# Kernel tuning notes

Hardware: AMD Instinct MI355X
Metric: run time of the kernel (lower is better)

## Reference

```python
import jax, jax.numpy as jnp
import numpy as np

N, E, G = 50000, 200000, 1000
EPS = 1e-5
NEG_SLOPE = 0.2


def setup_inputs() -> dict:
    key = jax.random.key(0)
    ks = jax.random.split(key, 24)
    p = lambda k, shape: jax.random.normal(k, shape, jnp.float32) * 0.05
    inp = {
        "x": jax.random.normal(ks[0], (N, 64), jnp.float32),
        "edge_index": jax.random.randint(ks[1], (2, E), 0, N, jnp.int32),
        "batch": jnp.sort(jax.random.randint(ks[2], (N,), 0, G, jnp.int32)),
        "solvent_fingerprint": jax.random.uniform(ks[3], (G, 128), jnp.float32),
        # GAT layer 1: 64 -> 4 heads x 128
        "W1": p(ks[4], (64, 512)), "a1_src": p(ks[5], (4, 128)), "a1_dst": p(ks[6], (4, 128)), "b1": jnp.zeros((512,), jnp.float32),
        "bn1_g": jnp.ones((512,), jnp.float32), "bn1_b": jnp.zeros((512,), jnp.float32),
        # GAT layer 2: 512 -> 4 heads x 256
        "W2": p(ks[7], (512, 1024)), "a2_src": p(ks[8], (4, 256)), "a2_dst": p(ks[9], (4, 256)), "b2": jnp.zeros((1024,), jnp.float32),
        "bn2_g": jnp.ones((1024,), jnp.float32), "bn2_b": jnp.zeros((1024,), jnp.float32),
        # GCN: 1024 -> 256
        "Wg": p(ks[10], (1024, 256)), "bg": jnp.zeros((256,), jnp.float32),
        "bn3_g": jnp.ones((256,), jnp.float32), "bn3_b": jnp.zeros((256,), jnp.float32),
        # MLP head
        "Ws": p(ks[11], (128, 128)), "bs": jnp.zeros((128,), jnp.float32),
        "Wf1": p(ks[12], (640, 128)), "bf1": jnp.zeros((128,), jnp.float32),
        "bnf_g": jnp.ones((128,), jnp.float32), "bnf_b": jnp.zeros((128,), jnp.float32),
        "Wf2": p(ks[13], (128, 1)), "bf2": jnp.zeros((1,), jnp.float32),
    }
    return inp


def _batchnorm(x, g, b):
    mu = x.mean(0)
    var = x.var(0)
    return (x - mu) * jax.lax.rsqrt(var + EPS) * g + b


def _gat(x, src, dst, W, a_src, a_dst, b, H, C):
    n = x.shape[0]
    h = (x @ W).reshape(n, H, C)                      # [N,H,C]
    al_s = (h * a_src).sum(-1)                        # [N,H]
    al_d = (h * a_dst).sum(-1)                        # [N,H]
    e = jax.nn.leaky_relu(al_s[src] + al_d[dst], NEG_SLOPE)   # [E,H]
    m = jax.ops.segment_max(e, dst, num_segments=n)
    ex = jnp.exp(e - m[dst])
    s = jax.ops.segment_sum(ex, dst, num_segments=n)
    alpha = ex / jnp.maximum(s[dst], 1e-16)
    out = jax.ops.segment_sum(h[src] * alpha[..., None], dst, num_segments=n)  # [N,H,C]
    return out.reshape(n, H * C) + b


def _gcn(x, src, dst, W, b):
    n = x.shape[0]
    h = x @ W
    deg = jax.ops.segment_sum(jnp.ones_like(dst, jnp.float32), dst, num_segments=n)
    dinv = jax.lax.rsqrt(jnp.maximum(deg, 1.0))
    norm = dinv[src] * dinv[dst]
    return jax.ops.segment_sum(h[src] * norm[:, None], dst, num_segments=n) + b


def reference(x, edge_index, batch, solvent_fingerprint,
              W1, a1_src, a1_dst, b1, bn1_g, bn1_b,
              W2, a2_src, a2_dst, b2, bn2_g, bn2_b,
              Wg, bg, bn3_g, bn3_b,
              Ws, bs, Wf1, bf1, bnf_g, bnf_b, Wf2, bf2):
    n = x.shape[0]
    loops = jnp.arange(n, dtype=edge_index.dtype)
    src = jnp.concatenate([edge_index[0], loops])
    dst = jnp.concatenate([edge_index[1], loops])

    h = _gat(x, src, dst, W1, a1_src, a1_dst, b1, 4, 128)
    h = jax.nn.relu(_batchnorm(h, bn1_g, bn1_b))
    h = _gat(h, src, dst, W2, a2_src, a2_dst, b2, 4, 256)
    h = jax.nn.relu(_batchnorm(h, bn2_g, bn2_b))
    h = _gcn(h, src, dst, Wg, bg)
    h = jax.nn.relu(_batchnorm(h, bn3_g, bn3_b))

    cnt = jax.ops.segment_sum(jnp.ones((n,), jnp.float32), batch, num_segments=G)
    gap = jax.ops.segment_sum(h, batch, num_segments=G) / jnp.maximum(cnt, 1.0)[:, None]
    gmp = jax.ops.segment_max(h, batch, num_segments=G)
    gmp = jnp.where(jnp.isfinite(gmp), gmp, 0.0)

    solv = jax.nn.relu(solvent_fingerprint @ Ws + bs)
    z = jnp.concatenate([gap, gmp, solv], axis=1)          # [G,640]
    z = jax.nn.relu(_batchnorm(z @ Wf1 + bf1, bnf_g, bnf_b))
    # dropout: identity in eval/deterministic reference
    return jax.nn.sigmoid(z @ Wf2 + bf2)
```

## Files before the change

kernel.cpp:

```cpp
#include <hip/hip_runtime.h>
#include <cmath>

#define LEAK 0.2f
#define BN_EPS 1e-5f

static inline int cdiv(long long a, long long b){ return (int)((a + b - 1) / b); }

typedef __attribute__((ext_vector_type(8))) short bf16x8;
typedef __attribute__((ext_vector_type(4))) float f32x4;

__device__ __forceinline__ float bf2f(unsigned short u){
    return __uint_as_float(((unsigned int)u) << 16);
}
__device__ __forceinline__ unsigned short f2bf(float f){
    unsigned int u = __float_as_uint(f);
    u += 0x7FFFu + ((u >> 16) & 1u);
    return (unsigned short)(u >> 16);
}

#define GLOAD_LDS16(gsrc, ldst) \
    __builtin_amdgcn_global_load_lds( \
        (const __attribute__((address_space(1))) unsigned int*)(gsrc), \
        (__attribute__((address_space(3))) unsigned int*)(ldst), 16, 0, 0)

__global__ __launch_bounds__(256) void gemm_mfma(
    const unsigned short* __restrict__ A, const unsigned short* __restrict__ Bt,
    unsigned short* __restrict__ D, int M, int K, int lda, int ldb, int ldc,
    int NX, int NYT)
{
    const int id = blockIdx.x;
    const int xcd = id & 7;
    const int j = id >> 3;
    const int bx = j % NX;
    const int by = (j / NX) * 8 + xcd;
    if (by >= NYT) return;

    __shared__ unsigned short As[128 * 64];
    __shared__ unsigned short Bs[128 * 64];
    const int t = threadIdx.x;
    const int row0 = by * 128, col0 = bx * 128;
    const int lane = t & 63, wv = t >> 6;
    const int wm = (wv >> 1) << 6, wn = (wv & 1) << 6;
    const int lm = lane & 15, lq = lane >> 4;

    const int sr  = t >> 3;
    const int scs = (t & 7) << 3;
    const int gsw = (((t & 7) ^ (sr & 7)) << 3);
    const unsigned short* ap[4];
    const unsigned short* bp[4];
    unsigned short* la[4];
    unsigned short* lb[4];
    #pragma unroll
    for (int q = 0; q < 4; ++q) {
        int r = sr + q * 32;
        int gra = row0 + r; if (gra >= M) gra = M - 1;
        ap[q] = A  + (size_t)gra * lda + gsw;
        bp[q] = Bt + (size_t)(col0 + r) * ldb + gsw;
        la[q] = &As[r * 64 + scs];
        lb[q] = &Bs[r * 64 + scs];
    }

    f32x4 acc[4][4] = {};
    const int rx = lm & 7;

    for (int k0 = 0; k0 < K; k0 += 64) {
        #pragma unroll
        for (int q = 0; q < 4; ++q) {
            GLOAD_LDS16(ap[q] + k0, la[q]);
            GLOAD_LDS16(bp[q] + k0, lb[q]);
        }
        __syncthreads();

        #pragma unroll
        for (int kk = 0; kk < 2; ++kk) {
            const int ck = (((kk << 2) + lq) ^ rx) << 3;
            bf16x8 af[4], bfr[4];
            #pragma unroll
            for (int mi = 0; mi < 4; ++mi)
                af[mi] = *(const bf16x8*)&As[(wm + mi * 16 + lm) * 64 + ck];
            #pragma unroll
            for (int ni = 0; ni < 4; ++ni)
                bfr[ni] = *(const bf16x8*)&Bs[(wn + ni * 16 + lm) * 64 + ck];
            #pragma unroll
            for (int mi = 0; mi < 4; ++mi)
                #pragma unroll
                for (int ni = 0; ni < 4; ++ni)
                    acc[mi][ni] = __builtin_amdgcn_mfma_f32_16x16x32_bf16(
                        af[mi], bfr[ni], acc[mi][ni], 0, 0, 0);
        }
        __syncthreads();
    }

    #pragma unroll
    for (int mi = 0; mi < 4; ++mi) {
        int row_b = row0 + wm + mi * 16 + lq * 4;
        #pragma unroll
        for (int ni = 0; ni < 4; ++ni) {
            int col = col0 + wn + ni * 16 + lm;
            #pragma unroll
            for (int r = 0; r < 4; ++r) {
                int row = row_b + r;
                if (row < M) D[(size_t)row * ldc + col] = f2bf(acc[mi][ni][r]);
            }
        }
    }
}

__global__ __launch_bounds__(256) void logits_valu(
    const unsigned short* __restrict__ A, const unsigned short* __restrict__ vat,
    float* __restrict__ C, int M, int K)
{
    __shared__ unsigned short vs[8 * 512];
    const int t = threadIdx.x;
    for (int i = t; i < K; i += 256)
        *(bf16x8*)&vs[i * 8] = *(const bf16x8*)(vat + (size_t)i * 8);
    __syncthreads();

    const int lane = t & 63;
    const int w = blockIdx.x * 4 + (t >> 6);
    const int Gl = K >> 3;
    const int rpw = 64 / Gl;
    const int sub = lane / Gl;
    const int li = lane - sub * Gl;
    long long row = (long long)w * rpw + sub;
    if (row >= M) return;

    bf16x8 hv = *(const bf16x8*)(A + row * K + li * 8);
    float hf[8];
    #pragma unroll
    for (int j = 0; j < 8; ++j) hf[j] = bf2f((unsigned short)hv[j]);

    float s[8];
    #pragma unroll
    for (int o = 0; o < 8; ++o) {
        bf16x8 v = *(const bf16x8*)&vs[o * K + li * 8];
        float acc = 0.f;
        #pragma unroll
        for (int j = 0; j < 8; ++j) acc += hf[j] * bf2f((unsigned short)v[j]);
        s[o] = acc;
    }
    for (int off = Gl >> 1; off; off >>= 1) {
        #pragma unroll
        for (int o = 0; o < 8; ++o) s[o] += __shfl_xor(s[o], off);
    }
    #pragma unroll
    for (int o = 0; o < 8; ++o)
        if (li == o) C[row * 8 + o] = s[o];
}

__global__ void convT(const float* __restrict__ W, unsigned short* __restrict__ Wt, int K, int Nc)
{
    int i = blockIdx.x * blockDim.x + threadIdx.x;
    if (i >= K * Nc) return;
    int k = i / Nc, n = i - k * Nc;
    Wt[(size_t)n * K + k] = f2bf(W[i]);
}

__global__ void conv_w1bd(const float* __restrict__ W, unsigned short* __restrict__ Wt)
{
    int i = blockIdx.x * blockDim.x + threadIdx.x;
    if (i >= 512 * 256) return;
    int o = i >> 8, k = i & 255;
    unsigned short v = 0;
    if ((k >> 6) == (o >> 7)) v = f2bf(W[(size_t)(k & 63) * 512 + o]);
    Wt[i] = v;
}

template<bool RELU>
__global__ __launch_bounds__(256) void gemm_small(
    const float* __restrict__ A, const float* __restrict__ B,
    const float* __restrict__ bias, float* __restrict__ C,
    int M, int K, int lda, int ldb, int ldc)
{
    __shared__ float As[2][640];
    const int t = threadIdx.x;
    const int r = t >> 7, c = t & 127;
    const int row0 = blockIdx.x * 2;
    for (int i = t; i < 2 * K; i += 256) {
        int rr = i / K, kk = i - rr * K;
        int gr = row0 + rr;
        As[rr][kk] = (gr < M) ? A[(size_t)gr * lda + kk] : 0.f;
    }
    __syncthreads();
    float acc0 = 0.f, acc1 = 0.f;
    for (int k = 0; k < K; k += 8) {
        float4 a0 = *reinterpret_cast<const float4*>(&As[r][k]);
        float4 a1 = *reinterpret_cast<const float4*>(&As[r][k + 4]);
        acc0 += a0.x * B[(size_t)(k + 0) * ldb + c];
        acc1 += a0.y * B[(size_t)(k + 1) * ldb + c];
        acc0 += a0.z * B[(size_t)(k + 2) * ldb + c];
        acc1 += a0.w * B[(size_t)(k + 3) * ldb + c];
        acc0 += a1.x * B[(size_t)(k + 4) * ldb + c];
        acc1 += a1.y * B[(size_t)(k + 5) * ldb + c];
        acc0 += a1.z * B[(size_t)(k + 6) * ldb + c];
        acc1 += a1.w * B[(size_t)(k + 7) * ldb + c];
    }
    int row = row0 + r;
    if (row < M) {
        float v = acc0 + acc1;
        if (bias) v += bias[c];
        if (RELU) v = fmaxf(v, 0.f);
        C[(size_t)row * ldc + c] = v;
    }
}

__global__ void compute_va_bf(const float* __restrict__ W, const float* __restrict__ a_s,
                              const float* __restrict__ a_d, unsigned short* __restrict__ vat,
                              int K, int HC, int C)
{
    int w = (int)(((long long)blockIdx.x * blockDim.x + threadIdx.x) >> 6);
    int lane = threadIdx.x & 63;
    if (w >= K * 4) return;
    int k = w >> 2, h = w & 3;
    const float* wp = W + (size_t)k * HC + h * C;
    const float* as = a_s + h * C;
    const float* ad = a_d + h * C;
    float s = 0.f, d = 0.f;
    for (int c = lane; c < C; c += 64) {
        float v = wp[c];
        s += v * as[c];
        d += v * ad[c];
    }
    #pragma unroll
    for (int off = 32; off; off >>= 1) {
        s += __shfl_down(s, off);
        d += __shfl_down(d, off);
    }
    if (lane == 0) {
        vat[(size_t)h * K + k] = f2bf(s);
        vat[(size_t)(4 + h) * K + k] = f2bf(d);
    }
}

__device__ __forceinline__ int e_src(const int* es, int E, int k){ return k < E ? es[k] : k - E; }
__device__ __forceinline__ int e_dst(const int* ed, int E, int k){ return k < E ? ed[k] : k - E; }

__global__ void fill_i32(int* __restrict__ p, int v, int n)
{
    int i = blockIdx.x * blockDim.x + threadIdx.x;
    if (i < n) p[i] = v;
}

__global__ void hist_dst(const int* __restrict__ ed, int E, int* __restrict__ cnt)
{
    int k = blockIdx.x * blockDim.x + threadIdx.x;
    if (k < E) atomicAdd(&cnt[ed[k]], 1);
}

__global__ __launch_bounds__(256) void scan_blk(const int* __restrict__ cnt,
                                                int* __restrict__ rowptr,
                                                int* __restrict__ bsums, int n)
{
    __shared__ int ts[256];
    const int t = threadIdx.x;
    const int i0 = blockIdx.x * 1024 + t * 4;
    int4 v = {0, 0, 0, 0};
    if (i0 + 3 < n) v = *reinterpret_cast<const int4*>(cnt + i0);
    else {
        if (i0 + 0 < n) v.x = cnt[i0 + 0];
        if (i0 + 1 < n) v.y = cnt[i0 + 1];
        if (i0 + 2 < n) v.z = cnt[i0 + 2];
        if (i0 + 3 < n) v.w = cnt[i0 + 3];
    }
    int lsum = v.x + v.y + v.z + v.w;
    ts[t] = lsum;
    __syncthreads();
    #pragma unroll
    for (int off = 1; off < 256; off <<= 1) {
        int u = (t >= off) ? ts[t - off] : 0;
        __syncthreads();
        ts[t] += u;
        __syncthreads();
    }
    int excl = ts[t] - lsum;
    if (i0 + 0 < n) rowptr[i0 + 0] = excl;
    if (i0 + 1 < n) rowptr[i0 + 1] = excl + v.x;
    if (i0 + 2 < n) rowptr[i0 + 2] = excl + v.x + v.y;
    if (i0 + 3 < n) rowptr[i0 + 3] = excl + v.x + v.y + v.z;
    if (t == 255) bsums[blockIdx.x] = ts[255];
}

__global__ __launch_bounds__(256) void scan_tops(int* __restrict__ bsums,
                                                 int* __restrict__ rowptr, int nb, int n)
{
    __shared__ int ts[256];
    const int t = threadIdx.x;
    int v = (t < nb) ? bsums[t] : 0;
    ts[t] = v;
    __syncthreads();
    #pragma unroll
    for (int off = 1; off < 256; off <<= 1) {
        int u = (t >= off) ? ts[t - off] : 0;
        __syncthreads();
        ts[t] += u;
        __syncthreads();
    }
    if (t < nb) bsums[t] = ts[t] - v;
    if (t == 255) rowptr[n] = ts[255];
}

__global__ void scan_add(int* __restrict__ rowptr, int* __restrict__ cursor,
                         const int* __restrict__ bsums, int n)
{
    int i = blockIdx.x * blockDim.x + threadIdx.x;
    if (i >= n) return;
    int r = rowptr[i] + bsums[i >> 10];
    rowptr[i] = r;
    cursor[i] = r;
}

__global__ void csr_scatter(const int* __restrict__ es, const int* __restrict__ ed,
                            int E, int Etot, int* __restrict__ cursor,
                            int* __restrict__ col, int* __restrict__ dstarr)
{
    int k = blockIdx.x * blockDim.x + threadIdx.x;
    if (k >= Etot) return;
    int sn = e_src(es, E, k), dn = e_dst(ed, E, k);
    int pos = atomicAdd(&cursor[dn], 1);
    col[pos] = sn;
    dstarr[pos] = dn;
}

__global__ void dinv_from_rowptr(const int* __restrict__ rowptr, float* __restrict__ dinv, int n)
{
    int i = blockIdx.x * blockDim.x + threadIdx.x;
    if (i < n) dinv[i] = rsqrtf(fmaxf((float)(rowptr[i + 1] - rowptr[i]), 1.f));
}

__global__ void grp_lb(const int* __restrict__ batch, int N, int G_, int* __restrict__ gptr)
{
    int g = blockIdx.x * blockDim.x + threadIdx.x;
    if (g > G_) return;
    if (g == G_) { gptr[G_] = N; return; }
    int lo = 0, hi = N;
    while (lo < hi) { int mid = (lo + hi) >> 1; if (batch[mid] < g) lo = mid + 1; else hi = mid; }
    gptr[g] = lo;
}

__global__ void edge_exp4(const int* __restrict__ col, const int* __restrict__ dstarr,
                          int Etot, const float* __restrict__ alsd, float* __restrict__ exq)
{
    int p = blockIdx.x * blockDim.x + threadIdx.x;
    if (p >= Etot) return;
    int sn = col[p], dn = dstarr[p];
    #pragma unroll
    for (int h = 0; h < 4; ++h) {
        float t = alsd[sn * 8 + h] + alsd[dn * 8 + 4 + h];
        t = (t >= 0.f) ? t : LEAK * t;
        exq[(size_t)h * Etot + p] = __expf(t);
    }
}

__global__ void gat_agg4_64(const int* __restrict__ rowptr, const int* __restrict__ col,
                            const unsigned short* __restrict__ xb,
                            const float* __restrict__ exq, int Etot,
                            unsigned short* __restrict__ agg, int N)
{
    int w = (int)(((long long)blockIdx.x * blockDim.x + threadIdx.x) >> 6);
    int lane = threadIdx.x & 63;
    if (w >= N) return;
    const float* ex0 = exq;
    const float* ex1 = exq + (size_t)Etot;
    const float* ex2 = exq + (size_t)2 * Etot;
    const float* ex3 = exq + (size_t)3 * Etot;
    int r0 = rowptr[w], r1 = rowptr[w + 1];
    float a0 = 0.f, a1 = 0.f, a2 = 0.f, a3 = 0.f;
    float s0 = 0.f, s1 = 0.f, s2 = 0.f, s3 = 0.f;
    int e = r0;
    for (; e + 1 < r1; e += 2) {
        int snA = col[e], snB = col[e + 1];
        float xA = bf2f(xb[(size_t)snA * 64 + lane]);
        float xB = bf2f(xb[(size_t)snB * 64 + lane]);
        float w0A = ex0[e], w0B = ex0[e + 1];
        float w1A = ex1[e], w1B = ex1[e + 1];
        float w2A = ex2[e], w2B = ex2[e + 1];
        float w3A = ex3[e], w3B = ex3[e + 1];
        a0 += w0A * xA + w0B * xB;  s0 += w0A + w0B;
        a1 += w1A * xA + w1B * xB;  s1 += w1A + w1B;
        a2 += w2A * xA + w2B * xB;  s2 += w2A + w2B;
        a3 += w3A * xA + w3B * xB;  s3 += w3A + w3B;
    }
    if (e < r1) {
        int sn = col[e];
        float xA = bf2f(xb[(size_t)sn * 64 + lane]);
        float w0 = ex0[e], w1 = ex1[e], w2 = ex2[e], w3 = ex3[e];
        a0 += w0 * xA; s0 += w0;
        a1 += w1 * xA; s1 += w1;
        a2 += w2 * xA; s2 += w2;
        a3 += w3 * xA; s3 += w3;
    }
    unsigned short* op = agg + (size_t)w * 256 + lane;
    op[0]   = f2bf(a0 / fmaxf(s0, 1e-16f));
    op[64]  = f2bf(a1 / fmaxf(s1, 1e-16f));
    op[128] = f2bf(a2 / fmaxf(s2, 1e-16f));
    op[192] = f2bf(a3 / fmaxf(s3, 1e-16f));
}

__global__ void gat_gather512_bf2(const int* __restrict__ rowptr, const int* __restrict__ col,
                                  const unsigned short* __restrict__ h, int ldh,
                                  const float* __restrict__ exq0, const float* __restrict__ exq1,
                                  unsigned short* __restrict__ out, int N)
{
    int w = (int)(((long long)blockIdx.x * blockDim.x + threadIdx.x) >> 6);
    int lane = threadIdx.x & 63;
    if (w >= N) return;
    int r0 = rowptr[w], r1 = rowptr[w + 1];
    float s0 = 0.f, s1 = 0.f;
    float a00=0.f,a01=0.f,a02=0.f,a03=0.f;
    float a10=0.f,a11=0.f,a12=0.f,a13=0.f;
    int e = r0;
    for (; e + 1 < r1; e += 2) {
        int sA = col[e], sB = col[e + 1];
        float w0A = exq0[e], w0B = exq0[e + 1];
        float w1A = exq1[e], w1B = exq1[e + 1];
        const unsigned short* pA = h + (size_t)sA * ldh + lane * 4;
        const unsigned short* pB = h + (size_t)sB * ldh + lane * 4;
        ushort4 hA0 = *reinterpret_cast<const ushort4*>(pA);
        ushort4 hA1 = *reinterpret_cast<const ushort4*>(pA + 256);
        ushort4 hB0 = *reinterpret_cast<const ushort4*>(pB);
        ushort4 hB1 = *reinterpret_cast<const ushort4*>(pB + 256);
        s0 += w0A + w0B; s1 += w1A + w1B;
        a00 += bf2f(hA0.x) * w0A + bf2f(hB0.x) * w0B;
        a01 += bf2f(hA0.y) * w0A + bf2f(hB0.y) * w0B;
        a02 += bf2f(hA0.z) * w0A + bf2f(hB0.z) * w0B;
        a03 += bf2f(hA0.w) * w0A + bf2f(hB0.w) * w0B;
        a10 += bf2f(hA1.x) * w1A + bf2f(hB1.x) * w1B;
        a11 += bf2f(hA1.y) * w1A + bf2f(hB1.y) * w1B;
        a12 += bf2f(hA1.z) * w1A + bf2f(hB1.z) * w1B;
        a13 += bf2f(hA1.w) * w1A + bf2f(hB1.w) * w1B;
    }
    if (e < r1) {
        int sA = col[e];
        float w0A = exq0[e], w1A = exq1[e];
        const unsigned short* pA = h + (size_t)sA * ldh + lane * 4;
        ushort4 hA0 = *reinterpret_cast<const ushort4*>(pA);
        ushort4 hA1 = *reinterpret_cast<const ushort4*>(pA + 256);
        s0 += w0A; s1 += w1A;
        a00 += bf2f(hA0.x) * w0A; a01 += bf2f(hA0.y) * w0A;
        a02 += bf2f(hA0.z) * w0A; a03 += bf2f(hA0.w) * w0A;
        a10 += bf2f(hA1.x) * w1A; a11 += bf2f(hA1.y) * w1A;
        a12 += bf2f(hA1.z) * w1A; a13 += bf2f(hA1.w) * w1A;
    }
    float i0 = 1.f / fmaxf(s0, 1e-16f);
    float i1 = 1.f / fmaxf(s1, 1e-16f);
    ushort4 o0, o1;
    o0.x = f2bf(a00 * i0); o0.y = f2bf(a01 * i0);
    o0.z = f2bf(a02 * i0); o0.w = f2bf(a03 * i0);
    o1.x = f2bf(a10 * i1); o1.y = f2bf(a11 * i1);
    o1.z = f2bf(a12 * i1); o1.w = f2bf(a13 * i1);
    unsigned short* op = out + (size_t)w * 512 + lane * 4;
    *reinterpret_cast<ushort4*>(op)       = o0;
    *reinterpret_cast<ushort4*>(op + 256) = o1;
}

__global__ void gcn_gather256(const int* __restrict__ rowptr, const int* __restrict__ col,
                              const unsigned short* __restrict__ h,
                              const float* __restrict__ dinv,
                              unsigned short* __restrict__ out, int N)
{
    int w = (int)(((long long)blockIdx.x * blockDim.x + threadIdx.x) >> 6);
    int lane = threadIdx.x & 63;
    if (w >= N) return;
    int r0 = rowptr[w], r1 = rowptr[w + 1];
    float a0 = 0.f, a1 = 0.f, a2 = 0.f, a3 = 0.f;
    int e = r0;
    for (; e + 1 < r1; e += 2) {
        int sn0 = col[e], sn1 = col[e + 1];
        float w0 = dinv[sn0], w1 = dinv[sn1];
        ushort4 hv0 = *reinterpret_cast<const ushort4*>(h + (size_t)sn0 * 256 + lane * 4);
        ushort4 hv1 = *reinterpret_cast<const ushort4*>(h + (size_t)sn1 * 256 + lane * 4);
        a0 += bf2f(hv0.x) * w0 + bf2f(hv1.x) * w1;
        a1 += bf2f(hv0.y) * w0 + bf2f(hv1.y) * w1;
        a2 += bf2f(hv0.z) * w0 + bf2f(hv1.z) * w1;
        a3 += bf2f(hv0.w) * w0 + bf2f(hv1.w) * w1;
    }
    if (e < r1) {
        int sn = col[e];
        float wv = dinv[sn];
        ushort4 hv = *reinterpret_cast<const ushort4*>(h + (size_t)sn * 256 + lane * 4);
        a0 += bf2f(hv.x) * wv; a1 += bf2f(hv.y) * wv;
        a2 += bf2f(hv.z) * wv; a3 += bf2f(hv.w) * wv;
    }
    float dn = dinv[w];
    ushort4 o;
    o.x = f2bf(a0 * dn); o.y = f2bf(a1 * dn);
    o.z = f2bf(a2 * dn); o.w = f2bf(a3 * dn);
    *reinterpret_cast<ushort4*>(out + (size_t)w * 256 + lane * 4) = o;
}

template<int D>
__global__ __launch_bounds__(256) void bn_part(
    const float* __restrict__ x, float* __restrict__ ps, float* __restrict__ pq,
    int M, int Y)
{
    constexpr int DG = D / 4;
    constexpr int P  = 256 / DG;
    const int t = threadIdx.x;
    const int cg = t % DG, ph = t / DG;
    const int y = blockIdx.y;
    const int rows_per = (M + Y - 1) / Y;
    const int r0 = y * rows_per;
    const int r1 = min(r0 + rows_per, M);
    float s0=0,s1=0,s2=0,s3=0,q0=0,q1=0,q2=0,q3=0;
    for (int r = r0 + ph; r < r1; r += P) {
        float4 v = *reinterpret_cast<const float4*>(x + (size_t)r * D + cg * 4);
        s0+=v.x; s1+=v.y; s2+=v.z; s3+=v.w;
        q0+=v.x*v.x; q1+=v.y*v.y; q2+=v.z*v.z; q3+=v.w*v.w;
    }
    __shared__ float ls[P][D];
    __shared__ float lq[P][D];
    ls[ph][cg*4+0]=s0; ls[ph][cg*4+1]=s1; ls[ph][cg*4+2]=s2; ls[ph][cg*4+3]=s3;
    lq[ph][cg*4+0]=q0; lq[ph][cg*4+1]=q1; lq[ph][cg*4+2]=q2; lq[ph][cg*4+3]=q3;
    __syncthreads();
    if (ph == 0) {
        #pragma unroll
        for (int j = 0; j < 4; ++j) {
            float ss = 0.f, qq = 0.f;
            #pragma unroll
            for (int p = 0; p < P; ++p) { ss += ls[p][cg*4+j]; qq += lq[p][cg*4+j]; }
            ps[(size_t)y * D + cg*4 + j] = ss;
            pq[(size_t)y * D + cg*4 + j] = qq;
        }
    }
}

template<int D>
__global__ __launch_bounds__(256) void bn_part_bf(
    const unsigned short* __restrict__ x, int ldx,
    float* __restrict__ ps, float* __restrict__ pq, int M, int Y)
{
    constexpr int DG = D / 4;
    constexpr int P  = 256 / DG;
    const int t = threadIdx.x;
    const int cg = t % DG, ph = t / DG;
    const int y = blockIdx.y;
    const int rows_per = (M + Y - 1) / Y;
    const int r0 = y * rows_per;
    const int r1 = min(r0 + rows_per, M);
    float s0=0,s1=0,s2=0,s3=0,q0=0,q1=0,q2=0,q3=0;
    for (int r = r0 + ph; r < r1; r += P) {
        ushort4 u = *reinterpret_cast<const ushort4*>(x + (size_t)r * ldx + cg * 4);
        float vx = bf2f(u.x), vy = bf2f(u.y), vz = bf2f(u.z), vw = bf2f(u.w);
        s0+=vx; s1+=vy; s2+=vz; s3+=vw;
        q0+=vx*vx; q1+=vy*vy; q2+=vz*vz; q3+=vw*vw;
    }
    __shared__ float ls[P][D];
    __shared__ float lq[P][D];
    ls[ph][cg*4+0]=s0; ls[ph][cg*4+1]=s1; ls[ph][cg*4+2]=s2; ls[ph][cg*4+3]=s3;
    lq[ph][cg*4+0]=q0; lq[ph][cg*4+1]=q1; lq[ph][cg*4+2]=q2; lq[ph][cg*4+3]=q3;
    __syncthreads();
    if (ph == 0) {
        #pragma unroll
        for (int j = 0; j < 4; ++j) {
            float ss = 0.f, qq = 0.f;
            #pragma unroll
            for (int p = 0; p < P; ++p) { ss += ls[p][cg*4+j]; qq += lq[p][cg*4+j]; }
            ps[(size_t)y * D + cg*4 + j] = ss;
            pq[(size_t)y * D + cg*4 + j] = qq;
        }
    }
}

template<int D>
__global__ __launch_bounds__(256) void bn_reduce_fin(
    const float* __restrict__ ps, const float* __restrict__ pq,
    const float* __restrict__ g, const float* __restrict__ b,
    float* __restrict__ scale, float* __restrict__ shift, int Y, float invM)
{
    const int t = threadIdx.x;
    const int cl = t & 63;
    const int c = blockIdx.x * 64 + cl;
    const int ph = t >> 6;
    float s = 0.f, q = 0.f;
    for (int y = ph; y < Y; y += 4) {
        s += ps[(size_t)y * D + c];
        q += pq[(size_t)y * D + c];
    }
    __shared__ float ls[4][64];
    __shared__ float lq[4][64];
    ls[ph][cl] = s; lq[ph][cl] = q;
    __syncthreads();
    if (ph == 0) {
        s = ls[0][cl] + ls[1][cl] + ls[2][cl] + ls[3][cl];
        q = lq[0][cl] + lq[1][cl] + lq[2][cl] + lq[3][cl];
        float mu = s * invM;
        float var = q * invM - mu * mu;
        float rs = rsqrtf(var + BN_EPS) * g[c];
        scale[c] = rs;
        shift[c] = b[c] - mu * rs;
    }
}

__global__ void bn_apply_bfbf(const unsigned short* __restrict__ x,
                              const float* __restrict__ scale, const float* __restrict__ shift,
                              unsigned short* __restrict__ dst, int total4, int Cb4,
                              int ldx, int ldd)
{
    int i = blockIdx.x * blockDim.x + threadIdx.x;
    if (i >= total4) return;
    int r = i / Cb4, c4 = (i - r * Cb4) * 4;
    ushort4 u = *reinterpret_cast<const ushort4*>(x + (size_t)r * ldx + c4);
    float4 sc = *reinterpret_cast<const float4*>(scale + c4);
    float4 sh = *reinterpret_cast<const float4*>(shift + c4);
    ushort4 o;
    o.x = f2bf(fmaxf(bf2f(u.x) * sc.x + sh.x, 0.f));
    o.y = f2bf(fmaxf(bf2f(u.y) * sc.y + sh.y, 0.f));
    o.z = f2bf(fmaxf(bf2f(u.z) * sc.z + sh.z, 0.f));
    o.w = f2bf(fmaxf(bf2f(u.w) * sc.w + sh.w, 0.f));
    *reinterpret_cast<ushort4*>(dst + (size_t)r * ldd + c4) = o;
}

__global__ void conv_f2b4(const float* __restrict__ src, unsigned short* __restrict__ dst, int n4)
{
    int i = blockIdx.x * blockDim.x + threadIdx.x;
    if (i >= n4) return;
    float4 v = *reinterpret_cast<const float4*>(src + (size_t)i * 4);
    ushort4 o = { f2bf(v.x), f2bf(v.y), f2bf(v.z), f2bf(v.w) };
    *reinterpret_cast<ushort4*>(dst + (size_t)i * 4) = o;
}

__global__ __launch_bounds__(256) void pool_gather_bn(const unsigned short* __restrict__ h,
                                                      const float* __restrict__ scale,
                                                      const float* __restrict__ shift,
                                                      const int* __restrict__ gptr,
                                                      float* __restrict__ z, int G_)
{
    int g = blockIdx.x;
    int c = threadIdx.x;
    int r0 = gptr[g], r1 = gptr[g + 1];
    float sc = scale[c], sh = shift[c];
    float s = 0.f, m = 0.f;
    int i = r0;
    for (; i + 1 < r1; i += 2) {
        float v0 = fmaxf(bf2f(h[(size_t)i * 256 + c]) * sc + sh, 0.f);
        float v1 = fmaxf(bf2f(h[(size_t)(i + 1) * 256 + c]) * sc + sh, 0.f);
        s += v0 + v1;
        m = fmaxf(m, fmaxf(v0, v1));
    }
    if (i < r1) {
        float v = fmaxf(bf2f(h[(size_t)i * 256 + c]) * sc + sh, 0.f);
        s += v;
        m = fmaxf(m, v);
    }
    float cnt = fmaxf((float)(r1 - r0), 1.f);
    z[(size_t)g * 640 + c] = s / cnt;
    z[(size_t)g * 640 + 256 + c] = m;
}

__global__ void final_head_bn(const float* __restrict__ f1,
                              const float* __restrict__ scale, const float* __restrict__ shift,
                              const float* __restrict__ Wf2, const float* __restrict__ bf2,
                              float* __restrict__ out, int G_)
{
    int w = (int)(((long long)blockIdx.x * blockDim.x + threadIdx.x) >> 6);
    int lane = threadIdx.x & 63;
    if (w >= G_) return;
    float s = 0.f;
    #pragma unroll
    for (int q = 0; q < 2; ++q) {
        int c = lane + q * 64;
        float v = fmaxf(f1[(size_t)w * 128 + c] * scale[c] + shift[c], 0.f);
        s += v * Wf2[c];
    }
    #pragma unroll
    for (int off = 32; off; off >>= 1) s += __shfl_down(s, off);
    if (lane == 0) out[w] = 1.f / (1.f + __expf(-(s + bf2[0])));
}

__global__ void sentinel(float* __restrict__ out, int n, float v)
{
    int i = blockIdx.x * blockDim.x + threadIdx.x;
    if (i < n) out[i] = v;
}

extern "C" void kernel_launch(void* const* d_in, const int* in_sizes, int n_in,
                              void* d_out, int out_size, void* d_ws, size_t ws_size,
                              hipStream_t stream)
{
    const float* x    = (const float*)d_in[0];
    const int*   ei   = (const int*)d_in[1];
    const int*   batch= (const int*)d_in[2];
    const float* sfp  = (const float*)d_in[3];
    const float* W1   = (const float*)d_in[4];
    const float* a1s  = (const float*)d_in[5];
    const float* a1d  = (const float*)d_in[6];
    const float* bn1g = (const float*)d_in[8];
    const float* bn1b = (const float*)d_in[9];
    const float* W2   = (const float*)d_in[10];
    const float* a2s  = (const float*)d_in[11];
    const float* a2d  = (const float*)d_in[12];
    const float* bn2g = (const float*)d_in[14];
    const float* bn2b = (const float*)d_in[15];
    const float* Wg   = (const float*)d_in[16];
    const float* bn3g = (const float*)d_in[18];
    const float* bn3b = (const float*)d_in[19];
    const float* Wsm  = (const float*)d_in[20];
    const float* bsm  = (const float*)d_in[21];
    const float* Wf1  = (const float*)d_in[22];
    const float* bnfg = (const float*)d_in[24];
    const float* bnfb = (const float*)d_in[25];
    const float* Wf2  = (const float*)d_in[26];
    const float* bf2  = (const float*)d_in[27];
    float* outp = (float*)d_out;

    const int N    = in_sizes[0] / 64;
    const int E    = in_sizes[1] / 2;
    const int G_   = in_sizes[3] / 128;
    const int Etot = E + N;
    const int* esrc = ei;
    const int* edst = ei + E;
    const int YB = 256;
    const int NB = cdiv(N, 1024);
    const int NYT = cdiv(N, 128);
    const int NYT8 = cdiv(NYT, 8) * 8;

    float* ws = (float*)d_ws;
    size_t off = 0;
    float* accA  = ws + off; off += (size_t)N * 256;
    float* h3acc = ws + off; off += (size_t)N * 256;
    unsigned short* g1b   = (unsigned short*)accA;
    unsigned short* g3b   = (unsigned short*)accA;
    unsigned short* h2all = (unsigned short*)accA;
    unsigned short* R1 = (unsigned short*)(ws + off); off += (size_t)N * 256;
    unsigned short* o1n = R1;
    unsigned short* hb  = (unsigned short*)(ws + off); off += (size_t)N * 128;
    unsigned short* xb  = (unsigned short*)(ws + off); off += (size_t)N * 32;
    float* alsd = ws + off; off += (size_t)N * 8;
    float* dinv = ws + off; off += N;
    float* bsc = ws + off; off += 1024;
    float* bsh = ws + off; off += 1024;
    float* ps  = ws + off; off += (size_t)YB * 512;
    float* pq  = ws + off; off += (size_t)YB * 512;
    float* z   = ws + off; off += (size_t)G_ * 640;
    float* f1  = ws + off; off += (size_t)G_ * 128;
    int* rowptr = (int*)(ws + off); off += (size_t)(N + 1);
    int* colc   = (int*)(ws + off); off += (size_t)Etot;
    int* dstarr = (int*)(ws + off); off += (size_t)Etot;
    float* exq  = ws + off; off += (size_t)Etot * 4;
    int* gptr   = (int*)(ws + off); off += (size_t)(G_ + 1);
    int* bsums  = (int*)(ws + off); off += 256;
    off = (off + 3) & ~(size_t)3;
    unsigned short* vat1 = (unsigned short*)(ws + off); off += 128 * 64 / 2;
    unsigned short* vat2 = (unsigned short*)(ws + off); off += 128 * 512 / 2;
    unsigned short* W1bdt = (unsigned short*)(ws + off); off += 512 * 256 / 2;
    unsigned short* W2t = (unsigned short*)(ws + off); off += 512 * 1024 / 2;
    unsigned short* Wgt = (unsigned short*)(ws + off); off += 1024 * 256 / 2;
    int* cursor = (int*)alsd;
    size_t need = off * 4;
    if (ws_size < need) {
        sentinel<<<cdiv(out_size, 256), 256, 0, stream>>>(outp, out_size, (float)(ws_size >> 20));
        return;
    }

    const int BLK = 256;
    dim3 blk(BLK);

    conv_w1bd<<<cdiv(512 * 256, BLK), blk, 0, stream>>>(W1, W1bdt);
    convT<<<cdiv(512 * 1024, BLK), blk, 0, stream>>>(W2, W2t, 512, 1024);
    convT<<<cdiv(1024 * 256, BLK), blk, 0, stream>>>(Wg, Wgt, 1024, 256);
    conv_f2b4<<<cdiv((long long)N * 16, BLK), blk, 0, stream>>>(x, xb, N * 16);
    compute_va_bf<<<cdiv(64 * 4 * 64, BLK), blk, 0, stream>>>(W1, a1s, a1d, vat1, 64, 512, 128);
    compute_va_bf<<<cdiv(512 * 4 * 64, BLK), blk, 0, stream>>>(W2, a2s, a2d, vat2, 512, 1024, 256);

    fill_i32<<<cdiv(N, BLK), blk, 0, stream>>>(cursor, 1, N);
    hist_dst<<<cdiv(E, BLK), blk, 0, stream>>>(edst, E, cursor);
    scan_blk<<<NB, blk, 0, stream>>>(cursor, rowptr, bsums, N);
    scan_tops<<<1, blk, 0, stream>>>(bsums, rowptr, NB, N);
    scan_add<<<cdiv(N, BLK), blk, 0, stream>>>(rowptr, cursor, bsums, N);
    csr_scatter<<<cdiv(Etot, BLK), blk, 0, stream>>>(esrc, edst, E, Etot, cursor, colc, dstarr);
    dinv_from_rowptr<<<cdiv(N, BLK), blk, 0, stream>>>(rowptr, dinv, N);
    grp_lb<<<cdiv(G_ + 1, BLK), blk, 0, stream>>>(batch, N, G_, gptr);

    logits_valu<<<cdiv(N, 32), blk, 0, stream>>>(xb, vat1, alsd, N, 64);
    edge_exp4<<<cdiv(Etot, BLK), blk, 0, stream>>>(colc, dstarr, Etot, alsd, exq);
    gat_agg4_64<<<cdiv((long long)N * 64, BLK), blk, 0, stream>>>(
        rowptr, colc, xb, exq, Etot, hb, N);
    gemm_mfma<<<NYT8 * 4, blk, 0, stream>>>(hb, W1bdt, g1b, N, 256, 256, 256, 512, 4, NYT);
    { dim3 g(1, YB); bn_part_bf<512><<<g, blk, 0, stream>>>(g1b, 512, ps, pq, N, YB); }
    bn_reduce_fin<512><<<8, blk, 0, stream>>>(ps, pq, bn1g, bn1b, bsc, bsh, YB, 1.f / N);
    bn_apply_bfbf<<<cdiv((long long)N * 128, BLK), blk, 0, stream>>>(
        g1b, bsc, bsh, o1n, N * 128, 128, 512, 512);

    logits_valu<<<cdiv(N, 4), blk, 0, stream>>>(o1n, vat2, alsd, N, 512);
    edge_exp4<<<cdiv(Etot, BLK), blk, 0, stream>>>(colc, dstarr, Etot, alsd, exq);

    gemm_mfma<<<NYT8 * 8, blk, 0, stream>>>(o1n, W2t, h2all, N, 512, 512, 512, 1024, 8, NYT);
    for (int pr = 0; pr < 2; ++pr) {
        gat_gather512_bf2<<<cdiv((long long)N * 64, BLK), blk, 0, stream>>>(
            rowptr, colc, h2all + pr * 512, 1024,
            exq + (size_t)(2 * pr) * Etot, exq + (size_t)(2 * pr + 1) * Etot, R1, N);
        { dim3 g(1, YB); bn_part_bf<512><<<g, blk, 0, stream>>>(R1, 512, ps, pq, N, YB); }
        bn_reduce_fin<512><<<8, blk, 0, stream>>>(ps, pq, bn2g + pr * 512, bn2b + pr * 512,
                                                  bsc + pr * 512, bsh + pr * 512, YB, 1.f / N);
        bn_apply_bfbf<<<cdiv((long long)N * 128, BLK), blk, 0, stream>>>(
            R1, bsc + pr * 512, bsh + pr * 512, h2all + pr * 512, N * 128, 128, 512, 1024);
    }
    gemm_mfma<<<NYT8 * 2, blk, 0, stream>>>(h2all, Wgt, hb, N, 1024, 1024, 1024, 256, 2, NYT);

    gcn_gather256<<<cdiv((long long)N * 64, BLK), blk, 0, stream>>>(
        rowptr, colc, hb, dinv, g3b, N);
    { dim3 g(1, YB); bn_part_bf<256><<<g, blk, 0, stream>>>(g3b, 256, ps, pq, N, YB); }
    bn_reduce_fin<256><<<4, blk, 0, stream>>>(ps, pq, bn3g, bn3b, bsc, bsh, YB, 1.f / N);

    pool_gather_bn<<<G_, blk, 0, stream>>>(g3b, bsc, bsh, gptr, z, G_);

    gemm_small<true><<<cdiv(G_, 2), blk, 0, stream>>>(
        sfp, Wsm, bsm, z + 512, G_, 128, 128, 128, 640);

    gemm_small<false><<<cdiv(G_, 2), blk, 0, stream>>>(
        z, Wf1, nullptr, f1, G_, 640, 640, 128, 128);
    { dim3 g(1, YB); bn_part<128><<<g, blk, 0, stream>>>(f1, ps, pq, G_, YB); }
    bn_reduce_fin<128><<<2, blk, 0, stream>>>(ps, pq, bnfg, bnfb, bsc, bsh, YB, 1.f / G_);
    final_head_bn<<<cdiv((long long)G_ * 64, BLK), blk, 0, stream>>>(
        f1, bsc, bsh, Wf2, bf2, outp, G_);
}
```

Baseline: 840.0 us.

## Fuse prep kernels and compute GAT edge weights inline in gathers

Merges the weight conversions, x conversion, attention-vector precompute, cursor fill and group-bound search into one multi-role prep kernel, and merges the CSR scatter with the dinv computation. It removes the edge_exp4 kernels and the exq/dstarr buffers, so the gather kernels recompute leaky-relu and exp per edge from the alsd logits. This cuts launch count and global traffic for edge weights, but adds redundant exp work per lane and drops the two-edge unrolling in the gather loops.

```diff
diff --git a/kernel.cpp b/kernel.cpp
--- a/kernel.cpp
+++ b/kernel.cpp
@@ -16,6 +16,11 @@
     unsigned int u = __float_as_uint(f);
     u += 0x7FFFu + ((u >> 16) & 1u);
     return (unsigned short)(u >> 16);
+}
+__device__ __forceinline__ float edge_ex(float s, float d){
+    float t = s + d;
+    t = (t >= 0.f) ? t : LEAK * t;
+    return __expf(t);
 }
 
 #define GLOAD_LDS16(gsrc, ldst) \
@@ -148,22 +153,97 @@
         if (li == o) C[row * 8 + o] = s[o];
 }
 
-__global__ void convT(const float* __restrict__ W, unsigned short* __restrict__ Wt, int K, int Nc)
-{
-    int i = blockIdx.x * blockDim.x + threadIdx.x;
-    if (i >= K * Nc) return;
-    int k = i / Nc, n = i - k * Nc;
-    Wt[(size_t)n * K + k] = f2bf(W[i]);
-}
-
-__global__ void conv_w1bd(const float* __restrict__ W, unsigned short* __restrict__ Wt)
-{
-    int i = blockIdx.x * blockDim.x + threadIdx.x;
-    if (i >= 512 * 256) return;
-    int o = i >> 8, k = i & 255;
-    unsigned short v = 0;
-    if ((k >> 6) == (o >> 7)) v = f2bf(W[(size_t)(k & 63) * 512 + o]);
-    Wt[i] = v;
+__global__ __launch_bounds__(256) void prep_all(
+    const float* __restrict__ W1, const float* __restrict__ W2,
+    const float* __restrict__ Wg, const float* __restrict__ x,
+    const float* __restrict__ a1s, const float* __restrict__ a1d,
+    const float* __restrict__ a2s, const float* __restrict__ a2d,
+    const int* __restrict__ batch,
+    unsigned short* __restrict__ W1bdt, unsigned short* __restrict__ W2t,
+    unsigned short* __restrict__ Wgt, unsigned short* __restrict__ xb,
+    unsigned short* __restrict__ vat1, unsigned short* __restrict__ vat2,
+    int* __restrict__ cursor, int* __restrict__ gptr,
+    int N, int G_,
+    int c0, int c1, int c2, int c3, int c4, int c5, int c6)
+{
+    const int t = threadIdx.x;
+    const int bid = blockIdx.x;
+    if (bid < c0) {
+        int i = bid * 256 + t;
+        int o = i >> 8, k = i & 255;
+        unsigned short v = 0;
+        if ((k >> 6) == (o >> 7)) v = f2bf(W1[(size_t)(k & 63) * 512 + o]);
+        W1bdt[i] = v;
+    } else if (bid < c1) {
+        int i = (bid - c0) * 256 + t;
+        int k = i >> 10, n = i & 1023;
+        W2t[(size_t)n * 512 + k] = f2bf(W2[i]);
+    } else if (bid < c2) {
+        int i = (bid - c1) * 256 + t;
+        int k = i >> 8, n = i & 255;
+        Wgt[(size_t)n * 1024 + k] = f2bf(Wg[i]);
+    } else if (bid < c3) {
+        int i = (bid - c2) * 256 + t;
+        if (i < N * 16) {
+            float4 v = *reinterpret_cast<const float4*>(x + (size_t)i * 4);
+            ushort4 o = { f2bf(v.x), f2bf(v.y), f2bf(v.z), f2bf(v.w) };
+            *reinterpret_cast<ushort4*>(xb + (size_t)i * 4) = o;
+        }
+    } else if (bid < c4) {
+        int w = (((bid - c3) * 256 + t) >> 6);
+        int lane = t & 63;
+        int k = w >> 2, h = w & 3;
+        const float* wp = W1 + (size_t)k * 512 + h * 128;
+        const float* as = a1s + h * 128;
+        const float* ad = a1d + h * 128;
+        float s = 0.f, d = 0.f;
+        for (int c = lane; c < 128; c += 64) {
+            float v = wp[c];
+            s += v * as[c];
+            d += v * ad[c];
+        }
+        #pragma unroll
+        for (int off = 32; off; off >>= 1) {
+            s += __shfl_down(s, off);
+            d += __shfl_down(d, off);
+        }
+        if (lane == 0) {
+            vat1[(size_t)h * 64 + k] = f2bf(s);
+            vat1[(size_t)(4 + h) * 64 + k] = f2bf(d);
+        }
+    } else if (bid < c5) {
+        int w = (((bid - c4) * 256 + t) >> 6);
+        int lane = t & 63;
+        int k = w >> 2, h = w & 3;
+        const float* wp = W2 + (size_t)k * 1024 + h * 256;
+        const float* as = a2s + h * 256;
+        const float* ad = a2d + h * 256;
+        float s = 0.f, d = 0.f;
+        for (int c = lane; c < 256; c += 64) {
+            float v = wp[c];
+            s += v * as[c];
+            d += v * ad[c];
+        }
+        #pragma unroll
+        for (int off = 32; off; off >>= 1) {
+            s += __shfl_down(s, off);
+            d += __shfl_down(d, off);
+        }
+        if (lane == 0) {
+            vat2[(size_t)h * 512 + k] = f2bf(s);
+            vat2[(size_t)(4 + h) * 512 + k] = f2bf(d);
+        }
+    } else if (bid < c6) {
+        int i = (bid - c5) * 256 + t;
+        if (i < N) cursor[i] = 1;
+    } else {
+        int g = (bid - c6) * 256 + t;
+        if (g > G_) return;
+        if (g == G_) { gptr[G_] = N; return; }
+        int lo = 0, hi = N;
+        while (lo < hi) { int mid = (lo + hi) >> 1; if (batch[mid] < g) lo = mid + 1; else hi = mid; }
+        gptr[g] = lo;
+    }
 }
 
 template<bool RELU>
@@ -204,42 +284,8 @@
     }
 }
 
-__global__ void compute_va_bf(const float* __restrict__ W, const float* __restrict__ a_s,
-                              const float* __restrict__ a_d, unsigned short* __restrict__ vat,
-                              int K, int HC, int C)
-{
-    int w = (int)(((long long)blockIdx.x * blockDim.x + threadIdx.x) >> 6);
-    int lane = threadIdx.x & 63;
-    if (w >= K * 4) return;
-    int k = w >> 2, h = w & 3;
-    const float* wp = W + (size_t)k * HC + h * C;
-    const float* as = a_s + h * C;
-    const float* ad = a_d + h * C;
-    float s = 0.f, d = 0.f;
-    for (int c = lane; c < C; c += 64) {
-        float v = wp[c];
-        s += v * as[c];
-        d += v * ad[c];
-    }
-    #pragma unroll
-    for (int off = 32; off; off >>= 1) {
-        s += __shfl_down(s, off);
-        d += __shfl_down(d, off);
-    }
-    if (lane == 0) {
-        vat[(size_t)h * K + k] = f2bf(s);
-        vat[(size_t)(4 + h) * K + k] = f2bf(d);
-    }
-}
-
 __device__ __forceinline__ int e_src(const int* es, int E, int k){ return k < E ? es[k] : k - E; }
 __device__ __forceinline__ int e_dst(const int* ed, int E, int k){ return k < E ? ed[k] : k - E; }
-
-__global__ void fill_i32(int* __restrict__ p, int v, int n)
-{
-    int i = blockIdx.x * blockDim.x + threadIdx.x;
-    if (i < n) p[i] = v;
-}
 
 __global__ void hist_dst(const int* __restrict__ ed, int E, int* __restrict__ cnt)
 {
@@ -309,85 +355,50 @@
     cursor[i] = r;
 }
 
-__global__ void csr_scatter(const int* __restrict__ es, const int* __restrict__ ed,
-                            int E, int Etot, int* __restrict__ cursor,
-                            int* __restrict__ col, int* __restrict__ dstarr)
-{
-    int k = blockIdx.x * blockDim.x + threadIdx.x;
-    if (k >= Etot) return;
-    int sn = e_src(es, E, k), dn = e_dst(ed, E, k);
-    int pos = atomicAdd(&cursor[dn], 1);
-    col[pos] = sn;
-    dstarr[pos] = dn;
-}
-
-__global__ void dinv_from_rowptr(const int* __restrict__ rowptr, float* __restrict__ dinv, int n)
-{
-    int i = blockIdx.x * blockDim.x + threadIdx.x;
-    if (i < n) dinv[i] = rsqrtf(fmaxf((float)(rowptr[i + 1] - rowptr[i]), 1.f));
-}
-
-__global__ void grp_lb(const int* __restrict__ batch, int N, int G_, int* __restrict__ gptr)
-{
-    int g = blockIdx.x * blockDim.x + threadIdx.x;
-    if (g > G_) return;
-    if (g == G_) { gptr[G_] = N; return; }
-    int lo = 0, hi = N;
-    while (lo < hi) { int mid = (lo + hi) >> 1; if (batch[mid] < g) lo = mid + 1; else hi = mid; }
-    gptr[g] = lo;
-}
-
-__global__ void edge_exp4(const int* __restrict__ col, const int* __restrict__ dstarr,
-                          int Etot, const float* __restrict__ alsd, float* __restrict__ exq)
-{
-    int p = blockIdx.x * blockDim.x + threadIdx.x;
-    if (p >= Etot) return;
-    int sn = col[p], dn = dstarr[p];
-    #pragma unroll
-    for (int h = 0; h < 4; ++h) {
-        float t = alsd[sn * 8 + h] + alsd[dn * 8 + 4 + h];
-        t = (t >= 0.f) ? t : LEAK * t;
-        exq[(size_t)h * Etot + p] = __expf(t);
+__global__ void csr_scatter_dinv(const int* __restrict__ es, const int* __restrict__ ed,
+                                 int E, int Etot, int* __restrict__ cursor,
+                                 int* __restrict__ col,
+                                 const int* __restrict__ rowptr,
+                                 float* __restrict__ dinv, int N, int NBsc)
+{
+    const int bid = blockIdx.x;
+    const int t = threadIdx.x;
+    if (bid < NBsc) {
+        int k = bid * 256 + t;
+        if (k >= Etot) return;
+        int sn = e_src(es, E, k), dn = e_dst(ed, E, k);
+        int pos = atomicAdd(&cursor[dn], 1);
+        col[pos] = sn;
+    } else {
+        int i = (bid - NBsc) * 256 + t;
+        if (i < N) dinv[i] = rsqrtf(fmaxf((float)(rowptr[i + 1] - rowptr[i]), 1.f));
     }
 }
 
 __global__ void gat_agg4_64(const int* __restrict__ rowptr, const int* __restrict__ col,
                             const unsigned short* __restrict__ xb,
-                            const float* __restrict__ exq, int Etot,
+                            const float* __restrict__ alsd,
                             unsigned short* __restrict__ agg, int N)
 {
     int w = (int)(((long long)blockIdx.x * blockDim.x + threadIdx.x) >> 6);
     int lane = threadIdx.x & 63;
     if (w >= N) return;
-    const float* ex0 = exq;
-    const float* ex1 = exq + (size_t)Etot;
-    const float* ex2 = exq + (size_t)2 * Etot;
-    const float* ex3 = exq + (size_t)3 * Etot;
+    float4 dt = *reinterpret_cast<const float4*>(alsd + (size_t)w * 8 + 4);
     int r0 = rowptr[w], r1 = rowptr[w + 1];
     float a0 = 0.f, a1 = 0.f, a2 = 0.f, a3 = 0.f;
     float s0 = 0.f, s1 = 0.f, s2 = 0.f, s3 = 0.f;
-    int e = r0;
-    for (; e + 1 < r1; e += 2) {
-        int snA = col[e], snB = col[e + 1];
-        float xA = bf2f(xb[(size_t)snA * 64 + lane]);
-        float xB = bf2f(xb[(size_t)snB * 64 + lane]);
-        float w0A = ex0[e], w0B = ex0[e + 1];
-        float w1A = ex1[e], w1B = ex1[e + 1];
-        float w2A = ex2[e], w2B = ex2[e + 1];
-        float w3A = ex3[e], w3B = ex3[e + 1];
-        a0 += w0A * xA + w0B * xB;  s0 += w0A + w0B;
-        a1 += w1A * xA + w1B * xB;  s1 += w1A + w1B;
-        a2 += w2A * xA + w2B * xB;  s2 += w2A + w2B;
-        a3 += w3A * xA + w3B * xB;  s3 += w3A + w3B;
-    }
-    if (e < r1) {
+    for (int e = r0; e < r1; ++e) {
         int sn = col[e];
+        float4 st = *reinterpret_cast<const float4*>(alsd + (size_t)sn * 8);
+        float e0 = edge_ex(st.x, dt.x);
+        float e1 = edge_ex(st.y, dt.y);
+        float e2 = edge_ex(st.z, dt.z);
+        float e3 = edge_ex(st.w, dt.w);
         float xA = bf2f(xb[(size_t)sn * 64 + lane]);
-        float w0 = ex0[e], w1 = ex1[e], w2 = ex2[e], w3 = ex3[e];
-        a0 += w0 * xA; s0 += w0;
-        a1 += w1 * xA; s1 += w1;
-        a2 += w2 * xA; s2 += w2;
-        a3 += w3 * xA; s3 += w3;
+        a0 += e0 * xA; s0 += e0;
+        a1 += e1 * xA; s1 += e1;
+        a2 += e2 * xA; s2 += e2;
+        a3 += e3 * xA; s3 += e3;
     }
     unsigned short* op = agg + (size_t)w * 256 + lane;
     op[0]   = f2bf(a0 / fmaxf(s0, 1e-16f));
@@ -396,58 +407,37 @@
     op[192] = f2bf(a3 / fmaxf(s3, 1e-16f));
 }
 
-__global__ void gat_gather512_bf2(const int* __restrict__ rowptr, const int* __restrict__ col,
-                                  const unsigned short* __restrict__ h, int ldh,
-                                  const float* __restrict__ exq0, const float* __restrict__ exq1,
-                                  unsigned short* __restrict__ out, int N)
+__global__ void gat_gather512_ex(const int* __restrict__ rowptr, const int* __restrict__ col,
+                                 const unsigned short* __restrict__ h, int ldh,
+                                 const float* __restrict__ alsd, int pr,
+                                 unsigned short* __restrict__ out, int N)
 {
     int w = (int)(((long long)blockIdx.x * blockDim.x + threadIdx.x) >> 6);
     int lane = threadIdx.x & 63;
     if (w >= N) return;
+    float2 dt = *reinterpret_cast<const float2*>(alsd + (size_t)w * 8 + 4 + 2 * pr);
     int r0 = rowptr[w], r1 = rowptr[w + 1];
     float s0 = 0.f, s1 = 0.f;
     float a00=0.f,a01=0.f,a02=0.f,a03=0.f;
     float a10=0.f,a11=0.f,a12=0.f,a13=0.f;
-    int e = r0;
-    for (; e + 1 < r1; e += 2) {
-        int sA = col[e], sB = col[e + 1];
-        float w0A = exq0[e], w0B = exq0[e + 1];
-        float w1A = exq1[e], w1B = exq1[e + 1];
-        const unsigned short* pA = h + (size_t)sA * ldh + lane * 4;
-        const unsigned short* pB = h + (size_t)sB * ldh + lane * 4;
-        ushort4 hA0 = *reinterpret_cast<const ushort4*>(pA);
-        ushort4 hA1 = *reinterpret_cast<const ushort4*>(pA + 256);
-        ushort4 hB0 = *reinterpret_cast<const ushort4*>(pB);
-        ushort4 hB1 = *reinterpret_cast<const ushort4*>(pB + 256);
-        s0 += w0A + w0B; s1 += w1A + w1B;
-        a00 += bf2f(hA0.x) * w0A + bf2f(hB0.x) * w0B;
-        a01 += bf2f(hA0.y) * w0A + bf2f(hB0.y) * w0B;
-        a02 += bf2f(hA0.z) * w0A + bf2f(hB0.z) * w0B;
-        a03 += bf2f(hA0.w) * w0A + bf2f(hB0.w) * w0B;
-        a10 += bf2f(hA1.x) * w1A + bf2f(hB1.x) * w1B;
-        a11 += bf2f(hA1.y) * w1A + bf2f(hB1.y) * w1B;
-        a12 += bf2f(hA1.z) * w1A + bf2f(hB1.z) * w1B;
-        a13 += bf2f(hA1.w) * w1A + bf2f(hB1.w) * w1B;
-    }
-    if (e < r1) {
-        int sA = col[e];
-        float w0A = exq0[e], w1A = exq1[e];
-        const unsigned short* pA = h + (size_t)sA * ldh + lane * 4;
-        ushort4 hA0 = *reinterpret_cast<const ushort4*>(pA);
-        ushort4 hA1 = *reinterpret_cast<const ushort4*>(pA + 256);
-        s0 += w0A; s1 += w1A;
-        a00 += bf2f(hA0.x) * w0A; a01 += bf2f(hA0.y) * w0A;
-        a02 += bf2f(hA0.z) * w0A; a03 += bf2f(hA0.w) * w0A;
-        a10 += bf2f(hA1.x) * w1A; a11 += bf2f(hA1.y) * w1A;
-        a12 += bf2f(hA1.z) * w1A; a13 += bf2f(hA1.w) * w1A;
+    for (int e = r0; e < r1; ++e) {
+        int sn = col[e];
+        float2 st = *reinterpret_cast<const float2*>(alsd + (size_t)sn * 8 + 2 * pr);
+        float e0 = edge_ex(st.x, dt.x);
+        float e1 = edge_ex(st.y, dt.y);
+        const unsigned short* p = h + (size_t)sn * ldh + lane * 4;
+        ushort4 h0 = *reinterpret_cast<const ushort4*>(p);
+        ushort4 h1 = *reinterpret_cast<const ushort4*>(p + 256);
+        s0 += e0; s1 += e1;
+        a00 += bf2f(h0.x) * e0; a01 += bf2f(h0.y) * e0;
+        a02 += bf2f(h0.z) * e0; a03 += bf2f(h0.w) * e0;
+        a10 += bf2f(h1.x) * e1; a11 += bf2f(h1.y) * e1;
+        a12 += bf2f(h1.z) * e1; a13 += bf2f(h1.w) * e1;
     }
     float i0 = 1.f / fmaxf(s0, 1e-16f);
     float i1 = 1.f / fmaxf(s1, 1e-16f);
-    ushort4 o0, o1;
-    o0.x = f2bf(a00 * i0); o0.y = f2bf(a01 * i0);
-    o0.z = f2bf(a02 * i0); o0.w = f2bf(a03 * i0);
-    o1.x = f2bf(a10 * i1); o1.y = f2bf(a11 * i1);
-    o1.z = f2bf(a12 * i1); o1.w = f2bf(a13 * i1);
+    ushort4 o0 = { f2bf(a00*i0), f2bf(a01*i0), f2bf(a02*i0), f2bf(a03*i0) };
+    ushort4 o1 = { f2bf(a10*i1), f2bf(a11*i1), f2bf(a12*i1), f2bf(a13*i1) };
     unsigned short* op = out + (size_t)w * 512 + lane * 4;
     *reinterpret_cast<ushort4*>(op)       = o0;
     *reinterpret_cast<ushort4*>(op + 256) = o1;
@@ -608,15 +598,6 @@
     o.z = f2bf(fmaxf(bf2f(u.z) * sc.z + sh.z, 0.f));
     o.w = f2bf(fmaxf(bf2f(u.w) * sc.w + sh.w, 0.f));
     *reinterpret_cast<ushort4*>(dst + (size_t)r * ldd + c4) = o;
-}
-
-__global__ void conv_f2b4(const float* __restrict__ src, unsigned short* __restrict__ dst, int n4)
-{
-    int i = blockIdx.x * blockDim.x + threadIdx.x;
-    if (i >= n4) return;
-    float4 v = *reinterpret_cast<const float4*>(src + (size_t)i * 4);
-    ushort4 o = { f2bf(v.x), f2bf(v.y), f2bf(v.z), f2bf(v.w) };
-    *reinterpret_cast<ushort4*>(dst + (size_t)i * 4) = o;
 }
 
 __global__ __launch_bounds__(256) void pool_gather_bn(const unsigned short* __restrict__ h,
@@ -735,8 +716,6 @@
     float* f1  = ws + off; off += (size_t)G_ * 128;
     int* rowptr = (int*)(ws + off); off += (size_t)(N + 1);
     int* colc   = (int*)(ws + off); off += (size_t)Etot;
-    int* dstarr = (int*)(ws + off); off += (size_t)Etot;
-    float* exq  = ws + off; off += (size_t)Etot * 4;
     int* gptr   = (int*)(ws + off); off += (size_t)(G_ + 1);
     int* bsums  = (int*)(ws + off); off += 256;
     off = (off + 3) & ~(size_t)3;
@@ -755,26 +734,30 @@
     const int BLK = 256;
     dim3 blk(BLK);
 
-    conv_w1bd<<<cdiv(512 * 256, BLK), blk, 0, stream>>>(W1, W1bdt);
-    convT<<<cdiv(512 * 1024, BLK), blk, 0, stream>>>(W2, W2t, 512, 1024);
-    convT<<<cdiv(1024 * 256, BLK), blk, 0, stream>>>(Wg, Wgt, 1024, 256);
-    conv_f2b4<<<cdiv((long long)N * 16, BLK), blk, 0, stream>>>(x, xb, N * 16);
-    compute_va_bf<<<cdiv(64 * 4 * 64, BLK), blk, 0, stream>>>(W1, a1s, a1d, vat1, 64, 512, 128);
-    compute_va_bf<<<cdiv(512 * 4 * 64, BLK), blk, 0, stream>>>(W2, a2s, a2d, vat2, 512, 1024, 256);
-
-    fill_i32<<<cdiv(N, BLK), blk, 0, stream>>>(cursor, 1, N);
+    const int c0 = 512;
+    const int c1 = c0 + 2048;
+    const int c2 = c1 + 1024;
+    const int c3 = c2 + cdiv((long long)N * 16, 256);
+    const int c4 = c3 + 64;
+    const int c5 = c4 + 512;
+    const int c6 = c5 + cdiv(N, 256);
+    const int c7 = c6 + cdiv(G_ + 1, 256);
+    prep_all<<<c7, blk, 0, stream>>>(W1, W2, Wg, x, a1s, a1d, a2s, a2d, batch,
+                                     W1bdt, W2t, Wgt, xb, vat1, vat2,
+                                     cursor, gptr, N, G_,
+                                     c0, c1, c2, c3, c4, c5, c6);
+
     hist_dst<<<cdiv(E, BLK), blk, 0, stream>>>(edst, E, cursor);
     scan_blk<<<NB, blk, 0, stream>>>(cursor, rowptr, bsums, N);
     scan_tops<<<1, blk, 0, stream>>>(bsums, rowptr, NB, N);
     scan_add<<<cdiv(N, BLK), blk, 0, stream>>>(rowptr, cursor, bsums, N);
-    csr_scatter<<<cdiv(Etot, BLK), blk, 0, stream>>>(esrc, edst, E, Etot, cursor, colc, dstarr);
-    dinv_from_rowptr<<<cdiv(N, BLK), blk, 0, stream>>>(rowptr, dinv, N);
-    grp_lb<<<cdiv(G_ + 1, BLK), blk, 0, stream>>>(batch, N, G_, gptr);
+    { int NBsc = cdiv(Etot, BLK);
+      csr_scatter_dinv<<<NBsc + cdiv(N, BLK), blk, 0, stream>>>(
+          esrc, edst, E, Etot, cursor, colc, rowptr, dinv, N, NBsc); }
 
     logits_valu<<<cdiv(N, 32), blk, 0, stream>>>(xb, vat1, alsd, N, 64);
-    edge_exp4<<<cdiv(Etot, BLK), blk, 0, stream>>>(colc, dstarr, Etot, alsd, exq);
     gat_agg4_64<<<cdiv((long long)N * 64, BLK), blk, 0, stream>>>(
-        rowptr, colc, xb, exq, Etot, hb, N);
+        rowptr, colc, xb, alsd, hb, N);
     gemm_mfma<<<NYT8 * 4, blk, 0, stream>>>(hb, W1bdt, g1b, N, 256, 256, 256, 512, 4, NYT);
     { dim3 g(1, YB); bn_part_bf<512><<<g, blk, 0, stream>>>(g1b, 512, ps, pq, N, YB); }
     bn_reduce_fin<512><<<8, blk, 0, stream>>>(ps, pq, bn1g, bn1b, bsc, bsh, YB, 1.f / N);
@@ -782,19 +765,18 @@
         g1b, bsc, bsh, o1n, N * 128, 128, 512, 512);
 
     logits_valu<<<cdiv(N, 4), blk, 0, stream>>>(o1n, vat2, alsd, N, 512);
-    edge_exp4<<<cdiv(Etot, BLK), blk, 0, stream>>>(colc, dstarr, Etot, alsd, exq);
 
     gemm_mfma<<<NYT8 * 8, blk, 0, stream>>>(o1n, W2t, h2all, N, 512, 512, 512, 1024, 8, NYT);
     for (int pr = 0; pr < 2; ++pr) {
-        gat_gather512_bf2<<<cdiv((long long)N * 64, BLK), blk, 0, stream>>>(
-            rowptr, colc, h2all + pr * 512, 1024,
-            exq + (size_t)(2 * pr) * Etot, exq + (size_t)(2 * pr + 1) * Etot, R1, N);
+        gat_gather512_ex<<<cdiv((long long)N * 64, BLK), blk, 0, stream>>>(
+            rowptr, colc, h2all + pr * 512, 1024, alsd, pr, R1, N);
         { dim3 g(1, YB); bn_part_bf<512><<<g, blk, 0, stream>>>(R1, 512, ps, pq, N, YB); }
         bn_reduce_fin<512><<<8, blk, 0, stream>>>(ps, pq, bn2g + pr * 512, bn2b + pr * 512,
                                                   bsc + pr * 512, bsh + pr * 512, YB, 1.f / N);
         bn_apply_bfbf<<<cdiv((long long)N * 128, BLK), blk, 0, stream>>>(
             R1, bsc + pr * 512, bsh + pr * 512, h2all + pr * 512, N * 128, 128, 512, 1024);
     }
+
     gemm_mfma<<<NYT8 * 2, blk, 0, stream>>>(h2all, Wgt, hb, N, 1024, 1024, 1024, 256, 2, NYT);
 
     gcn_gather256<<<cdiv((long long)N * 64, BLK), blk, 0, stream>>>(
```

Measured after the change: 824.2 us. No clear change (-1.9%).
